# Optimization experiments

Measured on AMD Instinct MI355X. Metric: run time of the kernel, lower is better.

The kernel has to match this reference:

```python
import jax, jax.numpy as jnp
import numpy as np

N = 100000
E = 1600000
F_IN = 256   # 4 * 64 after concat
H = 128

def _glorot(key, shape):
    fan_in, fan_out = shape
    lim = jnp.sqrt(6.0 / (fan_in + fan_out))
    return jax.random.uniform(key, shape, jnp.float32, -lim, lim)

def setup_inputs() -> dict:
    key = jax.random.key(0)
    ks = jax.random.split(key, 32)
    inp = {
        'x': jax.random.normal(ks[0], (N, 64), jnp.float32),
        'diff': jax.random.normal(ks[1], (N, 64), jnp.float32),
        'rec_prev': jax.random.normal(ks[2], (N, 64), jnp.float32),
        'hidden_prev': jax.random.normal(ks[3], (N, 64), jnp.float32),
        'edge_index': jax.random.randint(ks[4], (2, E), 0, N, jnp.int64),
    }
    dims = [(F_IN, H), (H, H), (H, H), (H, 1)]
    for i, (din, dout) in enumerate(dims):
        inp[f'Wl{i}'] = _glorot(ks[5 + 3 * i], (din, dout))  # neighbor (aggr) weight
        inp[f'Wr{i}'] = _glorot(ks[6 + 3 * i], (din, dout))  # root weight
        inp[f'b{i}'] = jnp.zeros((dout,), jnp.float32)
    return inp

def _sage_conv(h, src, dst, Wl, Wr, b):
    # mean aggregation of source-node features at destination nodes (PyG SAGEConv)
    msg_sum = jax.ops.segment_sum(h[src], dst, num_segments=N)        # [N, F]
    cnt = jax.ops.segment_sum(jnp.ones((src.shape[0],), h.dtype), dst, num_segments=N)
    mean = msg_sum / jnp.maximum(cnt, 1.0)[:, None]
    return mean @ Wl + h @ Wr + b

def reference(x, diff, rec_prev, hidden_prev, edge_index,
              Wl0, Wr0, b0, Wl1, Wr1, b1, Wl2, Wr2, b2, Wl3, Wr3, b3):
    src, dst = edge_index[0], edge_index[1]
    h = jnp.concatenate([x, diff, rec_prev, hidden_prev], axis=1)  # [N, 256]
    params = [(Wl0, Wr0, b0), (Wl1, Wr1, b1), (Wl2, Wr2, b2), (Wl3, Wr3, b3)]
    h = _sage_conv(h, src, dst, *params[0])
    for Wl, Wr, b in params[1:]:
        h = jax.nn.relu(h)
        h = _sage_conv(h, src, dst, Wl, Wr, b)
    out = jax.nn.sigmoid(h)          # [N, 1]
    lwp_util = jnp.mean(out)
    return out, lwp_util
```

## Files before the change

kernel.cpp:

```cpp
#include <hip/hip_runtime.h>
#include <hip/hip_bf16.h>

#define NN 100000
#define EE 1600000
#define HH 128
#define NB 391
#define CAP 5120
#define GB 1563
#define SB 256
#define EPB (EE / SB)
#define PPB 512
#define FB 6250
#define AB 6250

typedef short bf16x8 __attribute__((ext_vector_type(8)));
typedef short bf16x4 __attribute__((ext_vector_type(4)));
typedef float f32x4  __attribute__((ext_vector_type(4)));

__device__ inline short f2bf(float v) {
    __hip_bfloat16 b = __float2bfloat16(v);
    return *reinterpret_cast<short*>(&b);
}
__device__ inline float bf2f(short s) {
    unsigned int u = ((unsigned int)(unsigned short)s) << 16;
    return *reinterpret_cast<float*>(&u);
}

typedef __attribute__((address_space(1))) void gvoid_t;
typedef __attribute__((address_space(3))) void svoid_t;
__device__ __forceinline__ void gload16(const void* g, void* l) {
    __builtin_amdgcn_global_load_lds((gvoid_t*)g, (svoid_t*)l, 16, 0, 0);
}

__device__ __forceinline__ void ld_fence() { asm volatile("" ::: "memory"); }

template <int N>
__device__ __forceinline__ void wait_vm_bar() {
    if constexpr (N == 0)
        asm volatile("s_waitcnt vmcnt(0)\n\ts_barrier" ::: "memory");
    else if constexpr (N == 4)
        asm volatile("s_waitcnt vmcnt(4)\n\ts_barrier" ::: "memory");
    else if constexpr (N == 12)
        asm volatile("s_waitcnt vmcnt(12)\n\ts_barrier" ::: "memory");
    else if constexpr (N == 16)
        asm volatile("s_waitcnt vmcnt(16)\n\ts_barrier" ::: "memory");
    else if constexpr (N == 18)
        asm volatile("s_waitcnt vmcnt(18)\n\ts_barrier" ::: "memory");
    else
        static_assert(N == 0 || N == 4 || N == 12 || N == 16 || N == 18, "bad N");
}
__device__ __forceinline__ void barrier_only() {
    asm volatile("s_barrier" ::: "memory");
}

__global__ __launch_bounds__(256) void prep_scatter_kernel(
    const float* __restrict__ Wl0, const float* __restrict__ Wr0,
    const float* __restrict__ Wl1, const float* __restrict__ Wr1,
    const float* __restrict__ Wl2, const float* __restrict__ Wr2,
    __hip_bfloat16* __restrict__ WT0, __hip_bfloat16* __restrict__ WT1,
    __hip_bfloat16* __restrict__ WT2,
    const int* __restrict__ srcv, const int* __restrict__ dstv,
    int* __restrict__ bcur, int* __restrict__ pairs) {
    __shared__ int hist[NB];
    __shared__ int base[NB];
    const int t = threadIdx.x;

    if (blockIdx.x >= SB) {
        int id = (blockIdx.x - SB) * 256 + t;
        if (id < 65536) {
            int k = id & 255, n = id >> 8;
            float v = (n < 128) ? Wl0[(size_t)k * 128 + n]
                                : Wr0[(size_t)k * 128 + (n - 128)];
            WT0[(size_t)n * 256 + k] = __float2bfloat16(v);
        } else {
            id -= 65536;
            int layer = id >> 15;
            int u = id & 32767;
            int k = u & 127, n = u >> 7;
            const float* Wl = layer ? Wl2 : Wl1;
            const float* Wr = layer ? Wr2 : Wr1;
            __hip_bfloat16* WT = layer ? WT2 : WT1;
            float v = (n < 128) ? Wl[(size_t)k * 128 + n]
                                : Wr[(size_t)k * 128 + (n - 128)];
            WT[(size_t)n * 128 + k] = __float2bfloat16(v);
        }
        return;
    }

    for (int j = t; j < NB; j += 256) hist[j] = 0;
    __syncthreads();

    const int e0    = blockIdx.x * EPB;
    const int eend_ = e0 + EPB;

    for (int be = e0; be < eend_; be += 4096) {
        int d[16];
#pragma unroll
        for (int u = 0; u < 16; ++u) {
            const int e = be + u * 256 + t;
            d[u] = (e < eend_) ? dstv[e] : -1;
        }
#pragma unroll
        for (int u = 0; u < 16; ++u)
            if (d[u] >= 0) atomicAdd(&hist[d[u] >> 8], 1);
    }
    __syncthreads();

    for (int j = t; j < NB; j += 256)
        base[j] = hist[j] ? atomicAdd(&bcur[j], hist[j]) : 0;
    __syncthreads();
    for (int j = t; j < NB; j += 256) hist[j] = base[j];
    __syncthreads();

    for (int be = e0; be < eend_; be += 4096) {
        int s[16], d[16];
#pragma unroll
        for (int u = 0; u < 16; ++u) {
            const int e = be + u * 256 + t;
            if (e < eend_) { s[u] = srcv[e]; d[u] = dstv[e]; }
            else d[u] = -1;
        }
#pragma unroll
        for (int u = 0; u < 16; ++u)
            if (d[u] >= 0) {
                const int b   = d[u] >> 8;
                const int pos = atomicAdd(&hist[b], 1);
                if (pos < CAP) pairs[b * CAP + pos] = (s[u] << 8) | (d[u] & 255);
            }
    }
}

#define EW 264
template <int K, bool FIRST>
__device__ __forceinline__ void gemm_body(
    short* __restrict__ lsh, int bid,
    const __hip_bfloat16* hin,
    const float* __restrict__ x0, const float* __restrict__ x1,
    const float* __restrict__ x2, const float* __restrict__ x3,
    const __hip_bfloat16* __restrict__ wt, const float* __restrict__ bias,
    __hip_bfloat16* zout, __hip_bfloat16* __restrict__ rout) {
    const int t    = threadIdx.x;
    const int w    = t >> 6;
    const int lane = t & 63;
    const int quad = lane >> 4;
    const int l16  = lane & 15;
    const int n0   = bid * 64;

    constexpr int BUFB = FIRST ? 16384 : 8192;
    char* const lc = (char*)lsh;

    const __hip_bfloat16* afeat[4];
#pragma unroll
    for (int ft = 0; ft < 4; ++ft)
        afeat[ft] = wt + (size_t)(w * 64 + ft * 16 + l16) * K + quad * 8;

    f32x4 acc[4][4];
#pragma unroll
    for (int ft = 0; ft < 4; ++ft)
#pragma unroll
        for (int nt = 0; nt < 4; ++nt)
            acc[ft][nt] = (f32x4){0.f, 0.f, 0.f, 0.f};

    bf16x8 wreg[2][8];

    auto loadW = [&](int p, int pb) {
#pragma unroll
        for (int kcl = 0; kcl < 2; ++kcl)
#pragma unroll
            for (int ft = 0; ft < 4; ++ft)
                wreg[pb][kcl * 4 + ft] =
                    *(const bf16x8*)(afeat[ft] + (p * 2 + kcl) * 32);
    };

    auto stage = [&](int p, int bb) {
        char* lb = lc + bb * BUFB;
        if constexpr (FIRST) {
            const float* sp = (p == 0) ? x0 : (p == 1) ? x1 : (p == 2) ? x2 : x3;
#pragma unroll
            for (int i = 0; i < 4; ++i) {
                const int j   = w * 4 + i;
                const int row = j * 4 + (lane >> 4);
                int rg = n0 + row; if (rg > NN - 1) rg = NN - 1;
                const int colb = ((lane & 15) * 16) ^ ((row & 15) << 4);
                gload16((const char*)sp + (size_t)rg * 256 + colb, lb + j * 1024);
            }
        } else {
#pragma unroll
            for (int i = 0; i < 2; ++i) {
                const int j   = w * 2 + i;
                const int row = j * 8 + (lane >> 3);
                int rg = n0 + row; if (rg > NN - 1) rg = NN - 1;
                const int colb = ((lane & 7) * 16) ^ ((row & 7) << 4);
                gload16((const char*)hin + (size_t)rg * 256 + p * 128 + colb,
                        lb + j * 1024);
            }
        }
    };

    auto compute = [&](int s, int bb, int pb) {
        const char* lb = lc + bb * BUFB;
#pragma unroll
        for (int kcl = 0; kcl < 2; ++kcl) {
#pragma unroll
            for (int nt = 0; nt < 4; ++nt) {
                const int row = nt * 16 + l16;
                bf16x8 b;
                if constexpr (FIRST) {
                    const int sw = (row & 15) << 4;
                    const int B0 = kcl * 128 + quad * 32;
                    const char* rb = lb + row * 256;
                    const f32x4 lo = *(const f32x4*)(rb + ((B0) ^ sw));
                    const f32x4 hi = *(const f32x4*)(rb + ((B0 + 16) ^ sw));
                    b[0] = f2bf(lo[0]); b[1] = f2bf(lo[1]);
                    b[2] = f2bf(lo[2]); b[3] = f2bf(lo[3]);
                    b[4] = f2bf(hi[0]); b[5] = f2bf(hi[1]);
                    b[6] = f2bf(hi[2]); b[7] = f2bf(hi[3]);
                } else {
                    const int sw = (row & 7) << 4;
                    const int B0 = kcl * 64 + quad * 16;
                    b = *(const bf16x8*)(lb + row * 128 + (B0 ^ sw));
                }
#pragma unroll
                for (int ft = 0; ft < 4; ++ft)
                    acc[ft][nt] = __builtin_amdgcn_mfma_f32_16x16x32_bf16(
                        wreg[pb][kcl * 4 + ft], b, acc[ft][nt], 0, 0, 0);
            }
        }
    };

    if constexpr (FIRST) {
        loadW(0, 0); ld_fence();
        loadW(1, 1); ld_fence();
        stage(0, 0); ld_fence();
        stage(1, 1); ld_fence();
        wait_vm_bar<4>();
        compute(0, 0, 0); barrier_only();
        stage(2, 0); ld_fence(); loadW(2, 0); ld_fence();
        wait_vm_bar<12>();
        compute(1, 1, 1); barrier_only();
        stage(3, 1); ld_fence(); loadW(3, 1); ld_fence();
        wait_vm_bar<12>();
        compute(2, 0, 0); barrier_only();
        wait_vm_bar<0>();
        compute(3, 1, 1); barrier_only();
    } else {
        stage(0, 0); ld_fence();
        stage(1, 1); ld_fence();
        loadW(0, 0); loadW(1, 1);
        wait_vm_bar<18>(); compute(0, 0, 0); barrier_only();
        wait_vm_bar<16>(); compute(1, 1, 1); barrier_only();
    }

#pragma unroll
    for (int ft = 0; ft < 4; ++ft) {
        const int fb = ft * 16 + quad * 4;
        float4 bv = make_float4(0.f, 0.f, 0.f, 0.f);
        if (w >= 2) bv = *(const float4*)&bias[(w - 2) * 64 + fb];
        const int cbase = (w & 1) * 64 + ((w >= 2) ? 128 : 0);
#pragma unroll
        for (int nt = 0; nt < 4; ++nt) {
            const f32x4 a = acc[ft][nt];
            bf16x4 p;
            p[0] = f2bf(a[0] + bv.x); p[1] = f2bf(a[1] + bv.y);
            p[2] = f2bf(a[2] + bv.z); p[3] = f2bf(a[3] + bv.w);
            *(bf16x4*)&lsh[(nt * 16 + l16) * EW + cbase + fb] = p;
        }
    }
    __syncthreads();
#pragma unroll
    for (int u = 0; u < 8; ++u) {
        const int id  = u * 256 + t;
        const int row = id >> 5, ch = (id & 31) * 8;
        const int nd  = n0 + row;
        if (nd < NN) {
            const bf16x8 v = *(const bf16x8*)&lsh[row * EW + ch];
            if (ch < 128) *(bf16x8*)&zout[(size_t)nd * HH + ch] = v;
            else          *(bf16x8*)&rout[(size_t)nd * HH + (ch - 128)] = v;
        }
    }
}

template <int K>
__global__ __launch_bounds__(256) void gemm_kernel(
    const __hip_bfloat16* hin,
    const __hip_bfloat16* __restrict__ wt, const float* __restrict__ bias,
    __hip_bfloat16* zout, __hip_bfloat16* __restrict__ rout) {
    __shared__ short lsh[16896];
    gemm_body<K, false>(lsh, blockIdx.x, hin, nullptr, nullptr, nullptr, nullptr,
                        wt, bias, zout, rout);
}

__global__ __launch_bounds__(256) void fin_gemm0_kernel(
    const float* __restrict__ x0, const float* __restrict__ x1,
    const float* __restrict__ x2, const float* __restrict__ x3,
    const __hip_bfloat16* __restrict__ wt, const float* __restrict__ bias,
    __hip_bfloat16* __restrict__ zout, __hip_bfloat16* __restrict__ rout,
    const int* __restrict__ bcur, const int* __restrict__ pairs,
    int* __restrict__ csr, int* __restrict__ beg, int* __restrict__ eend,
    float* __restrict__ inv) {
    __shared__ short lsh[16896];
    const int t = threadIdx.x;

    if (blockIdx.x >= NB) {
        gemm_body<256, true>(lsh, blockIdx.x - NB, nullptr, x0, x1, x2, x3,
                             wt, bias, zout, rout);
        return;
    }

    int* cnt = (int*)lsh;
    int* scn = cnt + 256;
    int* cur = scn + 256;
    const int b = blockIdx.x;
    int m = bcur[b];
    if (m > CAP) m = CAP;

    cnt[t] = 0;
    __syncthreads();
    for (int e = t; e < m; e += 256)
        atomicAdd(&cnt[pairs[b * CAP + e] & 255], 1);
    __syncthreads();

    const int v = cnt[t];
    scn[t] = v;
    __syncthreads();
    for (int st = 1; st < 256; st <<= 1) {
        int tv = (t >= st) ? scn[t - st] : 0;
        __syncthreads();
        scn[t] += tv;
        __syncthreads();
    }
    const int myStart = scn[t] - v;
    cur[t] = myStart;
    __syncthreads();

    for (int e = t; e < m; e += 256) {
        const int pk  = pairs[b * CAP + e];
        const int pos = atomicAdd(&cur[pk & 255], 1);
        csr[b * CAP + pos] = pk >> 8;
    }

    const int node = b * 256 + t;
    if (node < NN) {
        beg[node]  = b * CAP + myStart;
        eend[node] = b * CAP + myStart + v;
        inv[node]  = 1.0f / fmaxf((float)v, 1.0f);
    }
}

template <bool LAST>
__global__ __launch_bounds__(256) void aggregate_kernel(
    const __hip_bfloat16* __restrict__ z, __hip_bfloat16* __restrict__ rio,
    const int* __restrict__ beg, const int* __restrict__ eend,
    const int* __restrict__ csr, const float* __restrict__ inv,
    const float* __restrict__ Wl3, const float* __restrict__ Wr3,
    const float* __restrict__ b3, float* __restrict__ z3,
    float* __restrict__ r3) {
    const int lane = threadIdx.x & 63;
    const int g    = lane >> 4;
    const int l16  = lane & 15;
    const int i    = ((blockIdx.x * 256 + threadIdx.x) >> 6) * 4 + g;
    if (i >= NN) return;
    const int b0 = beg[i], e0 = eend[i];
    const float iv = inv[i];
    const int  f   = l16 * 8;

    const bf16x8 rv8 = *(const bf16x8*)&rio[(size_t)i * HH + f];

    float acc[8];
#pragma unroll
    for (int j = 0; j < 8; ++j) acc[j] = 0.f;

    const size_t zoff = (size_t)f;
    int e = b0;
    for (; e + 7 < e0; e += 8) {
        int s[8];
#pragma unroll
        for (int u = 0; u < 8; ++u) s[u] = csr[e + u];
        bf16x8 zv[8];
#pragma unroll
        for (int u = 0; u < 8; ++u)
            zv[u] = *(const bf16x8*)&z[(size_t)s[u] * HH + zoff];
#pragma unroll
        for (int j = 0; j < 8; ++j) {
            float a0 = bf2f(zv[0][j]) + bf2f(zv[1][j]);
            float a1 = bf2f(zv[2][j]) + bf2f(zv[3][j]);
            float a2 = bf2f(zv[4][j]) + bf2f(zv[5][j]);
            float a3 = bf2f(zv[6][j]) + bf2f(zv[7][j]);
            acc[j] += (a0 + a1) + (a2 + a3);
        }
    }
    if (e + 3 < e0) {
        const int s0 = csr[e], s1 = csr[e + 1], s2 = csr[e + 2], s3 = csr[e + 3];
        const bf16x8 z0 = *(const bf16x8*)&z[(size_t)s0 * HH + zoff];
        const bf16x8 z1 = *(const bf16x8*)&z[(size_t)s1 * HH + zoff];
        const bf16x8 z2 = *(const bf16x8*)&z[(size_t)s2 * HH + zoff];
        const bf16x8 z3v = *(const bf16x8*)&z[(size_t)s3 * HH + zoff];
#pragma unroll
        for (int j = 0; j < 8; ++j)
            acc[j] += (bf2f(z0[j]) + bf2f(z1[j])) + (bf2f(z2[j]) + bf2f(z3v[j]));
        e += 4;
    }
    if (e < e0) {
        const int s0 = csr[e];
        const int s1 = (e + 1 < e0) ? csr[e + 1] : s0;
        const int s2 = (e + 2 < e0) ? csr[e + 2] : s0;
        const float m1 = (e + 1 < e0) ? 1.f : 0.f;
        const float m2 = (e + 2 < e0) ? 1.f : 0.f;
        const bf16x8 z0 = *(const bf16x8*)&z[(size_t)s0 * HH + zoff];
        const bf16x8 z1 = *(const bf16x8*)&z[(size_t)s1 * HH + zoff];
        const bf16x8 z2 = *(const bf16x8*)&z[(size_t)s2 * HH + zoff];
#pragma unroll
        for (int j = 0; j < 8; ++j) {
            acc[j] += bf2f(z0[j]);
            acc[j] = fmaf(m1, bf2f(z1[j]), acc[j]);
            acc[j] = fmaf(m2, bf2f(z2[j]), acc[j]);
        }
    }

    float ox[8];
    const __hip_bfloat162* rp = (const __hip_bfloat162*)&rv8;
#pragma unroll
    for (int j = 0; j < 4; ++j) {
        ox[2 * j]     = fmaxf(acc[2 * j]     * iv + __bfloat162float(rp[j].x), 0.f);
        ox[2 * j + 1] = fmaxf(acc[2 * j + 1] * iv + __bfloat162float(rp[j].y), 0.f);
    }

    if (!LAST) {
        bf16x8 o;
#pragma unroll
        for (int j = 0; j < 8; ++j) o[j] = f2bf(ox[j]);
        *(bf16x8*)&rio[(size_t)i * HH + f] = o;
    } else {
        const float4 wl0 = *(const float4*)&Wl3[f];
        const float4 wl1 = *(const float4*)&Wl3[f + 4];
        const float4 wr0 = *(const float4*)&Wr3[f];
        const float4 wr1 = *(const float4*)&Wr3[f + 4];
        float al = ox[0] * wl0.x + ox[1] * wl0.y + ox[2] * wl0.z + ox[3] * wl0.w
                 + ox[4] * wl1.x + ox[5] * wl1.y + ox[6] * wl1.z + ox[7] * wl1.w;
        float ar = ox[0] * wr0.x + ox[1] * wr0.y + ox[2] * wr0.z + ox[3] * wr0.w
                 + ox[4] * wr1.x + ox[5] * wr1.y + ox[6] * wr1.z + ox[7] * wr1.w;
#pragma unroll
        for (int m = 8; m; m >>= 1) {
            al += __shfl_xor(al, m, 64);
            ar += __shfl_xor(ar, m, 64);
        }
        if (l16 == 0) {
            z3[i] = al;
            r3[i] = ar + b3[0];
        }
    }
}

__global__ __launch_bounds__(256) void final_kernel(
    const float* __restrict__ z3, const float* __restrict__ r3,
    const int* __restrict__ beg, const int* __restrict__ eend,
    const int* __restrict__ csr, const float* __restrict__ inv,
    float* __restrict__ out, float* __restrict__ partial) {
    __shared__ float red[4];
    const int wv   = (blockIdx.x * 256 + threadIdx.x) >> 6;
    const int lane = threadIdx.x & 63;
    const int sub  = lane >> 4;
    const int l16  = lane & 15;
    const int w    = threadIdx.x >> 6;
    const int i    = wv * 4 + sub;
    float s = 0.f;
    if (i < NN) {
        const int b0 = beg[i], e0 = eend[i];
        float a = 0.f;
        for (int e = b0 + l16; e < e0; e += 16) a += z3[csr[e]];
        a += __shfl_xor(a, 1, 64);
        a += __shfl_xor(a, 2, 64);
        a += __shfl_xor(a, 4, 64);
        a += __shfl_xor(a, 8, 64);
        const float pre = a * inv[i] + r3[i];
        const float sg  = 1.f / (1.f + __expf(-pre));
        if (l16 == 0) { out[i] = sg; s = sg; }
    }
    s += __shfl_xor(s, 16, 64);
    s += __shfl_xor(s, 32, 64);
    if (lane == 0) red[w] = s;
    __syncthreads();
    if (threadIdx.x == 0)
        partial[blockIdx.x] = red[0] + red[1] + red[2] + red[3];
}

__global__ __launch_bounds__(256) void mean_kernel(const float* __restrict__ partial,
                                                   int nb, float* __restrict__ out) {
    __shared__ float lds[256];
    float s = 0.f;
    for (int i = threadIdx.x; i < nb; i += 256) s += partial[i];
    lds[threadIdx.x] = s;
    __syncthreads();
    for (int st = 128; st; st >>= 1) {
        if (threadIdx.x < st) lds[threadIdx.x] += lds[threadIdx.x + st];
        __syncthreads();
    }
    if (threadIdx.x == 0) out[NN] = lds[0] / (float)NN;
}

extern "C" void kernel_launch(void* const* d_in, const int* in_sizes, int n_in,
                              void* d_out, int out_size, void* d_ws, size_t ws_size,
                              hipStream_t stream) {
    const float* x    = (const float*)d_in[0];
    const float* diff = (const float*)d_in[1];
    const float* rec  = (const float*)d_in[2];
    const float* hid  = (const float*)d_in[3];
    const int* edge   = (const int*)d_in[4];
    const int* esrc = edge;
    const int* edst = edge + EE;
    const float* Wl0 = (const float*)d_in[5];
    const float* Wr0 = (const float*)d_in[6];
    const float* b0  = (const float*)d_in[7];
    const float* Wl1 = (const float*)d_in[8];
    const float* Wr1 = (const float*)d_in[9];
    const float* b1  = (const float*)d_in[10];
    const float* Wl2 = (const float*)d_in[11];
    const float* Wr2 = (const float*)d_in[12];
    const float* b2  = (const float*)d_in[13];
    const float* Wl3 = (const float*)d_in[14];
    const float* Wr3 = (const float*)d_in[15];
    const float* b3  = (const float*)d_in[16];
    float* out = (float*)d_out;

    char* w = (char*)d_ws;
    auto alloc = [&](size_t bytes) -> void* {
        void* p = (void*)w;
        w += (bytes + 255) & ~(size_t)255;
        return p;
    };
    __hip_bfloat16* bufA = (__hip_bfloat16*)alloc((size_t)NN * HH * 2);
    __hip_bfloat16* bufB = (__hip_bfloat16*)alloc((size_t)NN * HH * 2);
    __hip_bfloat16* WT0  = (__hip_bfloat16*)alloc((size_t)256 * 256 * 2);
    __hip_bfloat16* WT1  = (__hip_bfloat16*)alloc((size_t)256 * 128 * 2);
    __hip_bfloat16* WT2  = (__hip_bfloat16*)alloc((size_t)256 * 128 * 2);
    int*   pairs   = (int*)alloc((size_t)NB * CAP * 4);
    int*   csr     = (int*)alloc((size_t)NB * CAP * 4);
    int*   bcur    = (int*)alloc((size_t)512 * 4);
    int*   beg     = (int*)alloc((size_t)NN * 4);
    int*   eend    = (int*)alloc((size_t)NN * 4);
    float* inv     = (float*)alloc((size_t)NN * 4);
    float* z3      = (float*)alloc((size_t)NN * 4);
    float* r3      = (float*)alloc((size_t)NN * 4);
    float* partial = (float*)alloc((size_t)25000 * 4);

    hipMemsetAsync(bcur, 0, 512 * 4, stream);

    prep_scatter_kernel<<<SB + PPB, 256, 0, stream>>>(
        Wl0, Wr0, Wl1, Wr1, Wl2, Wr2, WT0, WT1, WT2,
        esrc, edst, bcur, pairs);

    fin_gemm0_kernel<<<NB + GB, 256, 0, stream>>>(
        x, diff, rec, hid, WT0, b0, bufA, bufB,
        bcur, pairs, csr, beg, eend, inv);

    aggregate_kernel<false><<<AB, 256, 0, stream>>>(bufA, bufB, beg, eend, csr, inv,
                                                    nullptr, nullptr, nullptr,
                                                    nullptr, nullptr);

    gemm_kernel<128><<<GB, 256, 0, stream>>>(bufB, WT1, b1, bufB, bufA);
    aggregate_kernel<false><<<AB, 256, 0, stream>>>(bufB, bufA, beg, eend, csr, inv,
                                                    nullptr, nullptr, nullptr,
                                                    nullptr, nullptr);

    gemm_kernel<128><<<GB, 256, 0, stream>>>(bufA, WT2, b2, bufA, bufB);
    aggregate_kernel<true><<<AB, 256, 0, stream>>>(bufA, bufB, beg, eend, csr, inv,
                                                   Wl3, Wr3, b3, z3, r3);

    final_kernel<<<FB, 256, 0, stream>>>(z3, r3, beg, eend, csr, inv, out, partial);
    mean_kernel<<<1, 256, 0, stream>>>(partial, FB, out);
}
```

Before: 454.0 us.

## Pre-convert concatenated fp32 inputs to bf16 and pipeline first-layer GEMM from it

Adds extra blocks to the prep kernel that convert the four fp32 input feature arrays into a single concatenated bf16 buffer. The first-layer GEMM then streams this bf16 buffer with a new three-buffer K=256 pipeline instead of loading fp32 directly. This halves the bytes the GEMM stage reads and lets it reuse the bf16 tile path. The cost is an extra write and read of 51 MB and a larger prep kernel. The old fp32 path stays as a fallback when workspace is too small.

```diff
diff --git a/kernel.cpp b/kernel.cpp
--- a/kernel.cpp
+++ b/kernel.cpp
@@ -10,6 +10,7 @@
 #define SB 256
 #define EPB (EE / SB)
 #define PPB 512
+#define CVB 6250
 #define FB 6250
 #define AB 6250
 
@@ -40,6 +41,10 @@
         asm volatile("s_waitcnt vmcnt(0)\n\ts_barrier" ::: "memory");
     else if constexpr (N == 4)
         asm volatile("s_waitcnt vmcnt(4)\n\ts_barrier" ::: "memory");
+    else if constexpr (N == 8)
+        asm volatile("s_waitcnt vmcnt(8)\n\ts_barrier" ::: "memory");
+    else if constexpr (N == 10)
+        asm volatile("s_waitcnt vmcnt(10)\n\ts_barrier" ::: "memory");
     else if constexpr (N == 12)
         asm volatile("s_waitcnt vmcnt(12)\n\ts_barrier" ::: "memory");
     else if constexpr (N == 16)
@@ -47,7 +52,8 @@
     else if constexpr (N == 18)
         asm volatile("s_waitcnt vmcnt(18)\n\ts_barrier" ::: "memory");
     else
-        static_assert(N == 0 || N == 4 || N == 12 || N == 16 || N == 18, "bad N");
+        static_assert(N == 0 || N == 4 || N == 8 || N == 10 || N == 12 ||
+                      N == 16 || N == 18, "bad N");
 }
 __device__ __forceinline__ void barrier_only() {
     asm volatile("s_barrier" ::: "memory");
@@ -59,11 +65,33 @@
     const float* __restrict__ Wl2, const float* __restrict__ Wr2,
     __hip_bfloat16* __restrict__ WT0, __hip_bfloat16* __restrict__ WT1,
     __hip_bfloat16* __restrict__ WT2,
+    const float* __restrict__ x0, const float* __restrict__ x1,
+    const float* __restrict__ x2, const float* __restrict__ x3,
+    __hip_bfloat16* __restrict__ xcat,
     const int* __restrict__ srcv, const int* __restrict__ dstv,
     int* __restrict__ bcur, int* __restrict__ pairs) {
     __shared__ int hist[NB];
     __shared__ int base[NB];
     const int t = threadIdx.x;
+
+    if (blockIdx.x >= SB + PPB) {
+        const int gid = (blockIdx.x - SB - PPB) * 256 + t;
+        const int a = gid / 400000;
+        const int u = gid - a * 400000;
+        const int n = u >> 2;
+        const int c = (u & 3) << 4;
+        const float* s = (a == 0) ? x0 : (a == 1) ? x1 : (a == 2) ? x2 : x3;
+        const float4* sp = (const float4*)(s + (size_t)n * 64 + c);
+        const float4 v0 = sp[0], v1 = sp[1], v2 = sp[2], v3 = sp[3];
+        bf16x8 o0, o1;
+        o0[0] = f2bf(v0.x); o0[1] = f2bf(v0.y); o0[2] = f2bf(v0.z); o0[3] = f2bf(v0.w);
+        o0[4] = f2bf(v1.x); o0[5] = f2bf(v1.y); o0[6] = f2bf(v1.z); o0[7] = f2bf(v1.w);
+        o1[0] = f2bf(v2.x); o1[1] = f2bf(v2.y); o1[2] = f2bf(v2.z); o1[3] = f2bf(v2.w);
+        o1[4] = f2bf(v3.x); o1[5] = f2bf(v3.y); o1[6] = f2bf(v3.z); o1[7] = f2bf(v3.w);
+        *(bf16x8*)&xcat[(size_t)n * 256 + a * 64 + c]     = o0;
+        *(bf16x8*)&xcat[(size_t)n * 256 + a * 64 + c + 8] = o1;
+        return;
+    }
 
     if (blockIdx.x >= SB) {
         int id = (blockIdx.x - SB) * 256 + t;
@@ -191,7 +219,7 @@
                 const int row = j * 8 + (lane >> 3);
                 int rg = n0 + row; if (rg > NN - 1) rg = NN - 1;
                 const int colb = ((lane & 7) * 16) ^ ((row & 7) << 4);
-                gload16((const char*)hin + (size_t)rg * 256 + p * 128 + colb,
+                gload16((const char*)hin + (size_t)rg * (K * 2) + p * 128 + colb,
                         lb + j * 1024);
             }
         }
@@ -243,6 +271,14 @@
         compute(2, 0, 0); barrier_only();
         wait_vm_bar<0>();
         compute(3, 1, 1); barrier_only();
+    } else if constexpr (K == 256) {
+        stage(0, 0); ld_fence();
+        stage(1, 1); ld_fence();
+        loadW(0, 0); ld_fence();
+        wait_vm_bar<10>(); loadW(1, 1); stage(2, 2); compute(0, 0, 0); barrier_only();
+        wait_vm_bar<18>(); loadW(2, 0); stage(3, 0); compute(1, 1, 1); barrier_only();
+        wait_vm_bar<10>(); loadW(3, 1);              compute(2, 2, 0); barrier_only();
+        wait_vm_bar<8>();                            compute(3, 0, 1); barrier_only();
     } else {
         stage(0, 0); ld_fence();
         stage(1, 1); ld_fence();
@@ -288,6 +324,67 @@
     __shared__ short lsh[16896];
     gemm_body<K, false>(lsh, blockIdx.x, hin, nullptr, nullptr, nullptr, nullptr,
                         wt, bias, zout, rout);
+}
+
+__device__ __forceinline__ void finalize_body(
+    short* lsh, int b, int t,
+    const int* __restrict__ bcur, const int* __restrict__ pairs,
+    int* __restrict__ csr, int* __restrict__ beg, int* __restrict__ eend,
+    float* __restrict__ inv) {
+    int* cnt = (int*)lsh;
+    int* scn = cnt + 256;
+    int* cur = scn + 256;
+    int m = bcur[b];
+    if (m > CAP) m = CAP;
+
+    cnt[t] = 0;
+    __syncthreads();
+    for (int e = t; e < m; e += 256)
+        atomicAdd(&cnt[pairs[b * CAP + e] & 255], 1);
+    __syncthreads();
+
+    const int v = cnt[t];
+    scn[t] = v;
+    __syncthreads();
+    for (int st = 1; st < 256; st <<= 1) {
+        int tv = (t >= st) ? scn[t - st] : 0;
+        __syncthreads();
+        scn[t] += tv;
+        __syncthreads();
+    }
+    const int myStart = scn[t] - v;
+    cur[t] = myStart;
+    __syncthreads();
+
+    for (int e = t; e < m; e += 256) {
+        const int pk  = pairs[b * CAP + e];
+        const int pos = atomicAdd(&cur[pk & 255], 1);
+        csr[b * CAP + pos] = pk >> 8;
+    }
+
+    const int node = b * 256 + t;
+    if (node < NN) {
+        beg[node]  = b * CAP + myStart;
+        eend[node] = b * CAP + myStart + v;
+        inv[node]  = 1.0f / fmaxf((float)v, 1.0f);
+    }
+}
+
+__global__ __launch_bounds__(256) void fin_gemm0b_kernel(
+    const __hip_bfloat16* __restrict__ xcat,
+    const __hip_bfloat16* __restrict__ wt, const float* __restrict__ bias,
+    __hip_bfloat16* __restrict__ zout, __hip_bfloat16* __restrict__ rout,
+    const int* __restrict__ bcur, const int* __restrict__ pairs,
+    int* __restrict__ csr, int* __restrict__ beg, int* __restrict__ eend,
+    float* __restrict__ inv) {
+    __shared__ short lsh[16896];
+    if (blockIdx.x >= NB) {
+        gemm_body<256, false>(lsh, blockIdx.x - NB, xcat,
+                              nullptr, nullptr, nullptr, nullptr,
+                              wt, bias, zout, rout);
+        return;
+    }
+    finalize_body(lsh, blockIdx.x, threadIdx.x, bcur, pairs, csr, beg, eend, inv);
 }
 
 __global__ __launch_bounds__(256) void fin_gemm0_kernel(
@@ -299,52 +396,12 @@
     int* __restrict__ csr, int* __restrict__ beg, int* __restrict__ eend,
     float* __restrict__ inv) {
     __shared__ short lsh[16896];
-    const int t = threadIdx.x;
-
     if (blockIdx.x >= NB) {
         gemm_body<256, true>(lsh, blockIdx.x - NB, nullptr, x0, x1, x2, x3,
                              wt, bias, zout, rout);
         return;
     }
-
-    int* cnt = (int*)lsh;
-    int* scn = cnt + 256;
-    int* cur = scn + 256;
-    const int b = blockIdx.x;
-    int m = bcur[b];
-    if (m > CAP) m = CAP;
-
-    cnt[t] = 0;
-    __syncthreads();
-    for (int e = t; e < m; e += 256)
-        atomicAdd(&cnt[pairs[b * CAP + e] & 255], 1);
-    __syncthreads();
-
-    const int v = cnt[t];
-    scn[t] = v;
-    __syncthreads();
-    for (int st = 1; st < 256; st <<= 1) {
-        int tv = (t >= st) ? scn[t - st] : 0;
-        __syncthreads();
-        scn[t] += tv;
-        __syncthreads();
-    }
-    const int myStart = scn[t] - v;
-    cur[t] = myStart;
-    __syncthreads();
-
-    for (int e = t; e < m; e += 256) {
-        const int pk  = pairs[b * CAP + e];
-        const int pos = atomicAdd(&cur[pk & 255], 1);
-        csr[b * CAP + pos] = pk >> 8;
-    }
-
-    const int node = b * 256 + t;
-    if (node < NN) {
-        beg[node]  = b * CAP + myStart;
-        eend[node] = b * CAP + myStart + v;
-        inv[node]  = 1.0f / fmaxf((float)v, 1.0f);
-    }
+    finalize_body(lsh, blockIdx.x, threadIdx.x, bcur, pairs, csr, beg, eend, inv);
 }
 
 template <bool LAST>
@@ -543,15 +600,25 @@
     float* r3      = (float*)alloc((size_t)NN * 4);
     float* partial = (float*)alloc((size_t)25000 * 4);
 
+    const size_t xcatBytes = (size_t)NN * 256 * 2;
+    const size_t used = (size_t)(w - (char*)d_ws);
+    const bool useCvt = (ws_size >= used + xcatBytes + (1u << 20));
+    __hip_bfloat16* xcat = useCvt ? (__hip_bfloat16*)alloc(xcatBytes) : nullptr;
+
     hipMemsetAsync(bcur, 0, 512 * 4, stream);
 
-    prep_scatter_kernel<<<SB + PPB, 256, 0, stream>>>(
+    const int g1 = SB + PPB + (useCvt ? CVB : 0);
+    prep_scatter_kernel<<<g1, 256, 0, stream>>>(
         Wl0, Wr0, Wl1, Wr1, Wl2, Wr2, WT0, WT1, WT2,
-        esrc, edst, bcur, pairs);
-
-    fin_gemm0_kernel<<<NB + GB, 256, 0, stream>>>(
-        x, diff, rec, hid, WT0, b0, bufA, bufB,
-        bcur, pairs, csr, beg, eend, inv);
+        x, diff, rec, hid, xcat, esrc, edst, bcur, pairs);
+
+    if (useCvt)
+        fin_gemm0b_kernel<<<NB + GB, 256, 0, stream>>>(
+            xcat, WT0, b0, bufA, bufB, bcur, pairs, csr, beg, eend, inv);
+    else
+        fin_gemm0_kernel<<<NB + GB, 256, 0, stream>>>(
+            x, diff, rec, hid, WT0, b0, bufA, bufB,
+            bcur, pairs, csr, beg, eend, inv);
 
     aggregate_kernel<false><<<AB, 256, 0, stream>>>(bufA, bufB, beg, eend, csr, inv,
                                                     nullptr, nullptr, nullptr,
```

After: 466.1 us. +2.7%, slower.
